# Optimization experiments

Hardware: AMD Instinct MI355X
Metric: run time of the kernel (lower is better)

## Reference

```python
import jax, jax.numpy as jnp
import numpy as np

F_, E_, B_, D_, H_, O_ = 4, 8, 4096, 512, 1024, 512


def setup_inputs() -> dict:
    key = jax.random.key(0)
    ks = jax.random.split(key, 7)
    s = 0.02  # small init scale to keep activations sane
    return {
        "features": jax.random.normal(ks[0], (F_, B_, D_), jnp.float32),
        "W1": jax.random.normal(ks[1], (F_, E_, D_, H_), jnp.float32) * s,
        "b1": jax.random.normal(ks[2], (F_, E_, H_), jnp.float32) * s,
        "W2": jax.random.normal(ks[3], (F_, E_, H_, O_), jnp.float32) * s,
        "b2": jax.random.normal(ks[4], (F_, E_, O_), jnp.float32) * s,
        "Wg": jax.random.normal(ks[5], (F_, D_, E_), jnp.float32) * s,
        "bg": jax.random.normal(ks[6], (F_, E_), jnp.float32) * s,
    }


def reference(features, W1, b1, W2, b2, Wg, bg):
    # Gate: softmax over experts, per feature. [F,B,E]
    gate = jax.nn.softmax(jnp.einsum('fbd,fde->fbe', features, Wg) + bg[:, None, :], axis=-1)
    # All experts computed densely (soft MoE): hidden [F,B,E,H]
    h = jax.nn.relu(jnp.einsum('fbd,fedh->fbeh', features, W1) + b1[:, None, :, :])
    # Expert outputs [F,B,E,O]
    eo = jnp.einsum('fbeh,feho->fbeo', h, W2) + b2[:, None, :, :]
    # Gate-weighted sum over experts, then mean over features -> [B,O]
    weighted = jnp.einsum('fbe,fbeo->fbo', gate, eo)
    return jnp.mean(weighted, axis=0)
```

## Files before the change

kernel.cpp:

```cpp
#include <hip/hip_runtime.h>


#define F_ 4
#define E_ 8
#define B_ 4096
#define D_ 512
#define H_ 1024
#define O_ 512

typedef unsigned short ushort_t;
typedef __bf16 bf16x8 __attribute__((ext_vector_type(8)));
typedef float f32x4 __attribute__((ext_vector_type(4)));
typedef unsigned short ushort8_t __attribute__((ext_vector_type(8)));

__device__ inline ushort_t f2bf(float f) {
  union { float f; unsigned u; } v; v.f = f;
  unsigned r = v.u + 0x7FFFu + ((v.u >> 16) & 1u);
  return (ushort_t)(r >> 16);
}
__device__ inline float bf2f(ushort_t u) {
  union { unsigned u; float f; } v; v.u = ((unsigned)u) << 16;
  return v.f;
}

__device__ inline void async16(const void* g, void* l) {
  __builtin_amdgcn_global_load_lds(
      (const __attribute__((address_space(1))) unsigned int*)g,
      (__attribute__((address_space(3))) unsigned int*)l, 16, 0, 0);
}

__device__ inline unsigned ldsOff(const void* p) {
  return (unsigned)(unsigned long long)(const __attribute__((address_space(3))) char*)p;
}
__device__ inline bf16x8 dsr128(unsigned byteOff) {
  bf16x8 r;
  asm volatile("ds_read_b128 %0, %1" : "=v"(r) : "v"(byteOff));
  return r;
}

#define VM0 asm volatile("s_waitcnt vmcnt(0)" ::: "memory")
#define VM6 asm volatile("s_waitcnt vmcnt(6)" ::: "memory")
#define BAR { __builtin_amdgcn_sched_barrier(0); __builtin_amdgcn_s_barrier(); \
              __builtin_amdgcn_sched_barrier(0); }

__global__ void prep_kernel(const float* __restrict__ features, const float* __restrict__ Wg,
                            const float* __restrict__ bg, float* __restrict__ g2,
                            ushort_t* __restrict__ featbf) {
  const int fb = blockIdx.x;
  const int f = fb >> 12, b = fb & (B_ - 1);
  const int lane = threadIdx.x;
  const float* feat = features + ((size_t)f * B_ + b) * D_;
  const float* wg = Wg + (size_t)f * D_ * E_;
  const int d0 = lane * 8;
  float ff[8];
  *(float4*)&ff[0] = *(const float4*)&feat[d0];
  *(float4*)&ff[4] = *(const float4*)&feat[d0 + 4];
  ushort8_t u;
#pragma unroll
  for (int k = 0; k < 8; ++k) u[k] = f2bf(ff[k]);
  *(ushort8_t*)&featbf[((size_t)f * B_ + b) * D_ + d0] = u;

  float acc[E_] = {0.f, 0.f, 0.f, 0.f, 0.f, 0.f, 0.f, 0.f};
#pragma unroll
  for (int k = 0; k < 8; ++k) {
    const float fv = ff[k];
    const float4 w0 = ((const float4*)(wg + (size_t)(d0 + k) * E_))[0];
    const float4 w1 = ((const float4*)(wg + (size_t)(d0 + k) * E_))[1];
    acc[0] += fv * w0.x; acc[1] += fv * w0.y; acc[2] += fv * w0.z; acc[3] += fv * w0.w;
    acc[4] += fv * w1.x; acc[5] += fv * w1.y; acc[6] += fv * w1.z; acc[7] += fv * w1.w;
  }
#pragma unroll
  for (int off = 32; off >= 1; off >>= 1)
#pragma unroll
    for (int e = 0; e < E_; ++e) acc[e] += __shfl_xor(acc[e], off, 64);
  float lg[E_], mx = -1e30f;
#pragma unroll
  for (int e = 0; e < E_; ++e) { lg[e] = acc[e] + bg[f * E_ + e]; mx = fmaxf(mx, lg[e]); }
  float s = 0.f;
#pragma unroll
  for (int e = 0; e < E_; ++e) { lg[e] = __expf(lg[e] - mx); s += lg[e]; }
  const float inv = 1.f / (s * (float)F_);
  if (lane < E_) g2[((size_t)f * B_ + b) * E_ + lane] = lg[lane] * inv;
}

__global__ void transpose_cast_kernel(const float* __restrict__ in, ushort_t* __restrict__ out,
                                      int R, int C) {
  __shared__ float tile[64][65];
  const size_t zoff = (size_t)blockIdx.z * R * C;
  in += zoff; out += zoff;
  const int tx = threadIdx.x & 63, ty = threadIdx.x >> 6;
  const int r0 = blockIdx.y * 64, c0 = blockIdx.x * 64;
#pragma unroll
  for (int i = 0; i < 16; ++i) {
    const int r = ty + i * 4;
    tile[r][tx] = in[(size_t)(r0 + r) * C + c0 + tx];
  }
  __syncthreads();
#pragma unroll
  for (int i = 0; i < 16; ++i) {
    const int c = ty + i * 4;
    out[(size_t)(c0 + c) * R + r0 + tx] = f2bf(tile[tx][c]);
  }
}


#define G1_STAGE(ktn, c) { \
    ushort_t* s_ = &lds[(c) * 32768]; \
    const ushort_t* a_ = aG + (ktn) * 64; \
    const ushort_t* b_ = bG + (ktn) * 64; \
    _Pragma("unroll") for (int p = 0; p < 4; ++p) { \
      async16(a_ + (size_t)p * (64 * D_), s_ + p * 4096 + t * 8); \
      async16(b_ + (size_t)p * (64 * D_), s_ + 16384 + p * 4096 + t * 8); } }

#define G1_PHASE(sb, kh) { \
    bf16x8 af[8], bfr[4]; \
    const unsigned cx = (unsigned)((((kh) * 4 + q) ^ (lr & 7)) * 16); \
    _Pragma("unroll") for (int i_ = 0; i_ < 8; ++i_) \
      af[i_] = dsr128((sb) + (unsigned)((wm * 128 + i_ * 16 + lr) * 128) + cx); \
    _Pragma("unroll") for (int j_ = 0; j_ < 4; ++j_) \
      bfr[j_] = dsr128((sb) + 32768u + (unsigned)((wn * 64 + j_ * 16 + lr) * 128) + cx); \
    asm volatile("s_waitcnt lgkmcnt(0)" ::: "memory"); \
    __builtin_amdgcn_sched_barrier(0); \
    __builtin_amdgcn_s_setprio(1); \
    _Pragma("unroll") for (int i_ = 0; i_ < 8; ++i_) \
      _Pragma("unroll") for (int j_ = 0; j_ < 4; ++j_) \
        acc[i_][j_] = __builtin_amdgcn_mfma_f32_16x16x32_bf16(bfr[j_], af[i_], acc[i_][j_], 0, 0, 0); \
    __builtin_amdgcn_s_setprio(0); \
    __builtin_amdgcn_sched_barrier(0); }

#define G1_ITER(kt, c) { \
    const unsigned sb = ldsB + (c) * 65536u; \
    G1_STAGE((kt) + 1, (c) ^ 1); \
    G1_PHASE(sb, 0); \
    G1_PHASE(sb, 1); \
    VM0; BAR; }

__global__ __launch_bounds__(512, 2) void gemm1_kernel(
    const ushort_t* __restrict__ featbf, const ushort_t* __restrict__ w1t,
    const float* __restrict__ b1, const float* __restrict__ g2,
    ushort_t* __restrict__ Hf, int f) {
  __shared__ __align__(16) ushort_t lds[65536];
  const int id = blockIdx.x;
  const int e = id & 7;
  const int s = id >> 3;
  const int n0 = (s & 3) * 256;
  const int m0 = (s >> 2) * 256;
  const ushort_t* A  = featbf + (size_t)f * B_ * D_;
  const ushort_t* Bp = w1t + ((size_t)f * E_ + e) * (size_t)H_ * D_;
  const float* b1e = b1 + ((size_t)f * E_ + e) * H_;
  const float* g2f = g2 + (size_t)f * B_ * E_;
  ushort_t* HfE = Hf + (size_t)e * B_ * H_;

  const int t = threadIdx.x, lane = t & 63, w = t >> 6;
  const int wm = w >> 2, wn = w & 3;
  const int lr = lane & 15, q = lane >> 4;
  const unsigned ldsB = ldsOff(lds);

  const int rr = t >> 3;
  const int cc = (t & 7) ^ (rr & 7);
  const ushort_t* aG = A  + (size_t)(m0 + rr) * D_ + cc * 8;
  const ushort_t* bG = Bp + (size_t)(n0 + rr) * D_ + cc * 8;

  f32x4 acc[8][4];
#pragma unroll
  for (int i = 0; i < 8; ++i)
#pragma unroll
    for (int j = 0; j < 4; ++j) acc[i][j] = (f32x4){0.f, 0.f, 0.f, 0.f};

  G1_STAGE(0, 0);
  VM0; BAR;

  G1_ITER(0, 0); G1_ITER(1, 1);
  G1_ITER(2, 0); G1_ITER(3, 1);
  G1_ITER(4, 0); G1_ITER(5, 1);
  G1_ITER(6, 0);
  { const unsigned sb = ldsB + 65536u;
    G1_PHASE(sb, 0); G1_PHASE(sb, 1); }

  __syncthreads();
  ushort_t* cb = lds;
#pragma unroll
  for (int mh = 0; mh < 2; ++mh) {
    if (wm == mh) {
#pragma unroll
      for (int i = 0; i < 8; ++i) {
        const int rl = i * 16 + lr;
        const float gv = g2f[(size_t)(m0 + mh * 128 + rl) * E_ + e];
#pragma unroll
        for (int j = 0; j < 4; ++j) {
          const int nl = wn * 64 + j * 16 + q * 4;
          const float4 bb = *(const float4*)&b1e[n0 + nl];
          ushort4 o;
          o.x = f2bf(fmaxf(acc[i][j][0] + bb.x, 0.f) * gv);
          o.y = f2bf(fmaxf(acc[i][j][1] + bb.y, 0.f) * gv);
          o.z = f2bf(fmaxf(acc[i][j][2] + bb.z, 0.f) * gv);
          o.w = f2bf(fmaxf(acc[i][j][3] + bb.w, 0.f) * gv);
          *(ushort4*)&cb[rl * 264 + nl] = o;
        }
      }
    }
    __syncthreads();
    const int row = t >> 2, seg = t & 3;
    const ushort_t* src = &cb[row * 264 + seg * 64];
    ushort_t* dst = HfE + (size_t)(m0 + mh * 128 + row) * H_ + n0 + seg * 64;
#pragma unroll
    for (int c2 = 0; c2 < 8; ++c2)
      *(ushort8_t*)(dst + c2 * 8) = *(const ushort8_t*)(src + c2 * 8);
    __syncthreads();
  }
}


#define G2_STAGE(ktn, c) { \
    ushort_t* s_ = &lds2[(c) * 24576]; \
    const ushort_t* a_ = Hf + (size_t)(e0 + ((ktn) >> 4)) * ((size_t)B_ * H_) + aOff + ((ktn) & 15) * 64; \
    const ushort_t* b_ = w2tF + (size_t)(e0 + ((ktn) >> 4)) * ((size_t)O_ * H_) + bOff + ((ktn) & 15) * 64; \
    _Pragma("unroll") for (int p = 0; p < 2; ++p) \
      async16(a_ + (size_t)p * (64 * H_), s_ + p * 4096 + t * 8); \
    _Pragma("unroll") for (int p = 0; p < 4; ++p) \
      async16(b_ + (size_t)p * (64 * H_), s_ + 8192 + p * 4096 + t * 8); }

#define G2_PHASE(sb, kh) { \
    bf16x8 af[4], bfr[4]; \
    const unsigned cx = (unsigned)((((kh) * 4 + q) ^ (lr & 7)) * 16); \
    _Pragma("unroll") for (int i_ = 0; i_ < 4; ++i_) \
      af[i_] = dsr128((sb) + (unsigned)((wm * 64 + i_ * 16 + lr) * 128) + cx); \
    _Pragma("unroll") for (int j_ = 0; j_ < 4; ++j_) \
      bfr[j_] = dsr128((sb) + 16384u + (unsigned)((wn * 64 + j_ * 16 + lr) * 128) + cx); \
    asm volatile("s_waitcnt lgkmcnt(0)" ::: "memory"); \
    __builtin_amdgcn_sched_barrier(0); \
    __builtin_amdgcn_s_setprio(1); \
    _Pragma("unroll") for (int i_ = 0; i_ < 4; ++i_) \
      _Pragma("unroll") for (int j_ = 0; j_ < 4; ++j_) \
        acc[i_][j_] = __builtin_amdgcn_mfma_f32_16x16x32_bf16(bfr[j_], af[i_], acc[i_][j_], 0, 0, 0); \
    __builtin_amdgcn_s_setprio(0); \
    __builtin_amdgcn_sched_barrier(0); }

#define G2_ITER(kt, c, cn) { \
    const unsigned sb = ldsB + (c) * 49152u; \
    G2_STAGE((kt) + 2, cn); \
    G2_PHASE(sb, 0); \
    G2_PHASE(sb, 1); \
    VM6; BAR; }

__global__ __launch_bounds__(512, 2) void gemm2_kernel(
    const ushort_t* __restrict__ Hf, const ushort_t* __restrict__ w2t,
    const float* __restrict__ b2, const float* __restrict__ g2,
    ushort_t* __restrict__ part, int f) {
  __shared__ __align__(16) ushort_t lds2[73728];
  const int id = blockIdx.x;
  const int grp = id & 3;
  const int s = id >> 2;
  const int n0 = (s & 1) * 256;
  const int m0 = (s >> 1) * 128;
  const int e0 = grp * 2;
  const ushort_t* w2tF = w2t + (size_t)f * E_ * O_ * H_;
  const float* g2f = g2 + (size_t)f * B_ * E_;

  const int t = threadIdx.x, lane = t & 63, w = t >> 6;
  const int wm = w >> 2, wn = w & 3;
  const int lr = lane & 15, q = lane >> 4;
  const unsigned ldsB = ldsOff(lds2);

  const int rr = t >> 3;
  const int cc = (t & 7) ^ (rr & 7);
  const size_t aOff = (size_t)(m0 + rr) * H_ + cc * 8;
  const size_t bOff = (size_t)(n0 + rr) * H_ + cc * 8;

  f32x4 acc[4][4];
#pragma unroll
  for (int i = 0; i < 4; ++i)
#pragma unroll
    for (int j = 0; j < 4; ++j) acc[i][j] = (f32x4){0.f, 0.f, 0.f, 0.f};

  G2_STAGE(0, 0); G2_STAGE(1, 1);
  VM6; BAR;

  for (int b = 0; b < 30; b += 3) {
    G2_ITER(b + 0, 0, 2);
    G2_ITER(b + 1, 1, 0);
    G2_ITER(b + 2, 2, 1);
  }
  { const unsigned sb = ldsB + 0u;
    G2_PHASE(sb, 0); G2_PHASE(sb, 1); VM0; BAR; }
  { const unsigned sb = ldsB + 49152u;
    G2_PHASE(sb, 0); G2_PHASE(sb, 1); }

  __syncthreads();
  ushort_t* cb = lds2;
  const float* b2e0 = b2 + ((size_t)f * E_ + e0) * O_;
  const float* b2e1 = b2e0 + O_;
#pragma unroll
  for (int i = 0; i < 4; ++i) {
    const int ml = wm * 64 + i * 16 + lr;
    const float gv0 = g2f[(size_t)(m0 + ml) * E_ + e0];
    const float gv1 = g2f[(size_t)(m0 + ml) * E_ + e0 + 1];
#pragma unroll
    for (int j = 0; j < 4; ++j) {
      const int nl = wn * 64 + j * 16 + q * 4;
      const int n = n0 + nl;
      const float4 c0 = *(const float4*)&b2e0[n];
      const float4 c1 = *(const float4*)&b2e1[n];
      ushort4 o;
      o.x = f2bf(acc[i][j][0] + gv0 * c0.x + gv1 * c1.x);
      o.y = f2bf(acc[i][j][1] + gv0 * c0.y + gv1 * c1.y);
      o.z = f2bf(acc[i][j][2] + gv0 * c0.z + gv1 * c1.z);
      o.w = f2bf(acc[i][j][3] + gv0 * c0.w + gv1 * c1.w);
      *(ushort4*)&cb[ml * 264 + nl] = o;
    }
  }
  __syncthreads();
  const int row = t >> 2, seg = t & 3;
  const ushort_t* src = &cb[row * 264 + seg * 64];
  ushort_t* dst = part + (size_t)(f * 4 + grp) * (B_ * O_) + (size_t)(m0 + row) * O_ + n0 + seg * 64;
#pragma unroll
  for (int c2 = 0; c2 < 8; ++c2)
    *(ushort8_t*)(dst + c2 * 8) = *(const ushort8_t*)(src + c2 * 8);
}

__global__ void reduce_kernel(const ushort_t* __restrict__ part, float* __restrict__ out) {
  const size_t p = ((size_t)blockIdx.x * 256 + threadIdx.x) * 8;
  float s[8] = {0.f, 0.f, 0.f, 0.f, 0.f, 0.f, 0.f, 0.f};
#pragma unroll
  for (int k = 0; k < F_ * 4; ++k) {
    const ushort8_t u = *(const ushort8_t*)&part[(size_t)k * (B_ * O_) + p];
#pragma unroll
    for (int j = 0; j < 8; ++j) s[j] += bf2f(u[j]);
  }
  float4 o0 = {s[0], s[1], s[2], s[3]}, o1 = {s[4], s[5], s[6], s[7]};
  *(float4*)&out[p] = o0;
  *(float4*)&out[p + 4] = o1;
}

extern "C" void kernel_launch(void* const* d_in, const int* in_sizes, int n_in,
                              void* d_out, int out_size, void* d_ws, size_t ws_size,
                              hipStream_t stream) {
  const float* features = (const float*)d_in[0];
  const float* W1 = (const float*)d_in[1];
  const float* b1 = (const float*)d_in[2];
  const float* W2 = (const float*)d_in[3];
  const float* b2 = (const float*)d_in[4];
  const float* Wg = (const float*)d_in[5];
  const float* bg = (const float*)d_in[6];
  float* out = (float*)d_out;

  char* ws = (char*)d_ws;
  ushort_t* featbf = (ushort_t*)ws;
  ushort_t* w1t    = (ushort_t*)(ws + 16777216);
  ushort_t* w2t    = (ushort_t*)(ws + 50331648);
  float*    g2     = (float*)(ws + 83886080);
  ushort_t* Hf     = (ushort_t*)(ws + 84410368);
  ushort_t* part   = (ushort_t*)(ws + 151519232);

  prep_kernel<<<F_ * B_, 64, 0, stream>>>(features, Wg, bg, g2, featbf);
  transpose_cast_kernel<<<dim3(H_ / 64, D_ / 64, F_ * E_), 256, 0, stream>>>(W1, w1t, D_, H_);
  transpose_cast_kernel<<<dim3(O_ / 64, H_ / 64, F_ * E_), 256, 0, stream>>>(W2, w2t, H_, O_);

  for (int f = 0; f < F_; ++f) {
    gemm1_kernel<<<512, 512, 0, stream>>>(featbf, w1t, b1, g2, Hf, f);
    gemm2_kernel<<<256, 512, 0, stream>>>(Hf, w2t, b2, g2, part, f);
  }
  reduce_kernel<<<B_ * O_ / 8 / 256, 256, 0, stream>>>(part, out);
}
```

Measured before the change: 621.6 us.

## Restructure GEMM pipelines into half-K phases with per-phase staging and new warp layout

Both GEMM kernels now load K in 32-wide half-tiles. Each half-tile gets its own async stage and a barrier before it is read, and the next stage's loads are issued between the LDS reads and the MFMAs. Partial vmcnt waits replace the full drains. The warp grid changes from 2x4 to 4x2, the LDS swizzle is rebuilt for 64-byte rows, and gemm2's block tile goes from 128x256 to 256x128 with a smaller LDS footprint. The aim is finer-grained overlap of global loads with compute and less LDS, in exchange for more barriers per K step.

```diff
diff --git a/kernel.cpp b/kernel.cpp
--- a/kernel.cpp
+++ b/kernel.cpp
@@ -38,10 +38,12 @@
   return r;
 }
 
+#define LGKM0 asm volatile("s_waitcnt lgkmcnt(0)" ::: "memory")
+#define VM4 asm volatile("s_waitcnt vmcnt(4)" ::: "memory")
+#define VM3 asm volatile("s_waitcnt vmcnt(3)" ::: "memory")
 #define VM0 asm volatile("s_waitcnt vmcnt(0)" ::: "memory")
-#define VM6 asm volatile("s_waitcnt vmcnt(6)" ::: "memory")
-#define BAR { __builtin_amdgcn_sched_barrier(0); __builtin_amdgcn_s_barrier(); \
-              __builtin_amdgcn_sched_barrier(0); }
+#define SCB __builtin_amdgcn_sched_barrier(0)
+#define SBAR __builtin_amdgcn_s_barrier()
 
 __global__ void prep_kernel(const float* __restrict__ features, const float* __restrict__ Wg,
                             const float* __restrict__ bg, float* __restrict__ g2,
@@ -104,36 +106,28 @@
 }
 
 
-#define G1_STAGE(ktn, c) { \
-    ushort_t* s_ = &lds[(c) * 32768]; \
-    const ushort_t* a_ = aG + (ktn) * 64; \
-    const ushort_t* b_ = bG + (ktn) * 64; \
-    _Pragma("unroll") for (int p = 0; p < 4; ++p) { \
-      async16(a_ + (size_t)p * (64 * D_), s_ + p * 4096 + t * 8); \
-      async16(b_ + (size_t)p * (64 * D_), s_ + 16384 + p * 4096 + t * 8); } }
-
-#define G1_PHASE(sb, kh) { \
-    bf16x8 af[8], bfr[4]; \
-    const unsigned cx = (unsigned)((((kh) * 4 + q) ^ (lr & 7)) * 16); \
-    _Pragma("unroll") for (int i_ = 0; i_ < 8; ++i_) \
-      af[i_] = dsr128((sb) + (unsigned)((wm * 128 + i_ * 16 + lr) * 128) + cx); \
-    _Pragma("unroll") for (int j_ = 0; j_ < 4; ++j_) \
-      bfr[j_] = dsr128((sb) + 32768u + (unsigned)((wn * 64 + j_ * 16 + lr) * 128) + cx); \
-    asm volatile("s_waitcnt lgkmcnt(0)" ::: "memory"); \
-    __builtin_amdgcn_sched_barrier(0); \
+#define STG1(ktn, kh) { \
+    char* d_ = (char*)lds + (((ktn) & 1) << 16) + (kh) * 16384 + t * 16; \
+    const int ko_ = (ktn) * 64 + (kh) * 32; \
+    async16(aT + ko_, d_); \
+    async16(aT + 128 * D_ + ko_, d_ + 8192); \
+    async16(bT + ko_, d_ + 32768); \
+    async16(bT + 128 * D_ + ko_, d_ + 40960); }
+
+#define PH1(kt, kh, DOSTG, VMS) { \
+    VMS; \
+    asm volatile("" ::: "memory"); SBAR; SCB; \
+    const unsigned sb_ = ldsB + (unsigned)(((kt) & 1) << 16) + (kh) * 16384u; \
+    bf16x8 af[4], bfr[8]; \
+    _Pragma("unroll") for (int i_ = 0; i_ < 4; ++i_) af[i_] = dsr128(sb_ + aRd + i_ * 1024u); \
+    _Pragma("unroll") for (int j_ = 0; j_ < 8; ++j_) bfr[j_] = dsr128(sb_ + 32768u + bRd + j_ * 1024u); \
+    if (DOSTG) { STG1((kt) + 1, kh); } \
+    LGKM0; SCB; \
     __builtin_amdgcn_s_setprio(1); \
-    _Pragma("unroll") for (int i_ = 0; i_ < 8; ++i_) \
-      _Pragma("unroll") for (int j_ = 0; j_ < 4; ++j_) \
+    _Pragma("unroll") for (int i_ = 0; i_ < 4; ++i_) \
+      _Pragma("unroll") for (int j_ = 0; j_ < 8; ++j_) \
         acc[i_][j_] = __builtin_amdgcn_mfma_f32_16x16x32_bf16(bfr[j_], af[i_], acc[i_][j_], 0, 0, 0); \
-    __builtin_amdgcn_s_setprio(0); \
-    __builtin_amdgcn_sched_barrier(0); }
-
-#define G1_ITER(kt, c) { \
-    const unsigned sb = ldsB + (c) * 65536u; \
-    G1_STAGE((kt) + 1, (c) ^ 1); \
-    G1_PHASE(sb, 0); \
-    G1_PHASE(sb, 1); \
-    VM0; BAR; }
+    __builtin_amdgcn_s_setprio(0); SCB; }
 
 __global__ __launch_bounds__(512, 2) void gemm1_kernel(
     const ushort_t* __restrict__ featbf, const ushort_t* __restrict__ w1t,
@@ -145,50 +139,50 @@
   const int s = id >> 3;
   const int n0 = (s & 3) * 256;
   const int m0 = (s >> 2) * 256;
-  const ushort_t* A  = featbf + (size_t)f * B_ * D_;
-  const ushort_t* Bp = w1t + ((size_t)f * E_ + e) * (size_t)H_ * D_;
   const float* b1e = b1 + ((size_t)f * E_ + e) * H_;
   const float* g2f = g2 + (size_t)f * B_ * E_;
   ushort_t* HfE = Hf + (size_t)e * B_ * H_;
 
   const int t = threadIdx.x, lane = t & 63, w = t >> 6;
-  const int wm = w >> 2, wn = w & 3;
+  const int wm = w >> 1, wn = w & 1;
   const int lr = lane & 15, q = lane >> 4;
   const unsigned ldsB = ldsOff(lds);
-
-  const int rr = t >> 3;
-  const int cc = (t & 7) ^ (rr & 7);
-  const ushort_t* aG = A  + (size_t)(m0 + rr) * D_ + cc * 8;
-  const ushort_t* bG = Bp + (size_t)(n0 + rr) * D_ + cc * 8;
-
-  f32x4 acc[8][4];
-#pragma unroll
-  for (int i = 0; i < 8; ++i)
-#pragma unroll
-    for (int j = 0; j < 4; ++j) acc[i][j] = (f32x4){0.f, 0.f, 0.f, 0.f};
-
-  G1_STAGE(0, 0);
-  VM0; BAR;
-
-  G1_ITER(0, 0); G1_ITER(1, 1);
-  G1_ITER(2, 0); G1_ITER(3, 1);
-  G1_ITER(4, 0); G1_ITER(5, 1);
-  G1_ITER(6, 0);
-  { const unsigned sb = ldsB + 65536u;
-    G1_PHASE(sb, 0); G1_PHASE(sb, 1); }
-
-  __syncthreads();
+  const unsigned csw = (unsigned)((q ^ ((lr >> 1) & 3)) << 4);
+  const unsigned aRd = (unsigned)((wm * 64 + lr) * 64) + csw;
+  const unsigned bRd = (unsigned)((wn * 128 + lr) * 64) + csw;
+
+  const int cc = (t & 3) ^ ((t >> 3) & 3);
+  const ushort_t* aT = featbf + (size_t)f * B_ * D_ + (size_t)(m0 + (t >> 2)) * D_ + cc * 8;
+  const ushort_t* bT = w1t + ((size_t)f * E_ + e) * ((size_t)H_ * D_) +
+                       (size_t)(n0 + (t >> 2)) * D_ + cc * 8;
+
+  f32x4 acc[4][8];
+#pragma unroll
+  for (int i = 0; i < 4; ++i)
+#pragma unroll
+    for (int j = 0; j < 8; ++j) acc[i][j] = (f32x4){0.f, 0.f, 0.f, 0.f};
+
+  STG1(0, 0); STG1(0, 1);
+
+  for (int kt = 0; kt < 7; ++kt) {
+    PH1(kt, 0, true, VM4);
+    PH1(kt, 1, true, VM4);
+  }
+  PH1(7, 0, false, VM4);
+  PH1(7, 1, false, VM0);
+
+  asm volatile("" ::: "memory"); SBAR; SCB;
   ushort_t* cb = lds;
 #pragma unroll
   for (int mh = 0; mh < 2; ++mh) {
-    if (wm == mh) {
-#pragma unroll
-      for (int i = 0; i < 8; ++i) {
-        const int rl = i * 16 + lr;
+    if ((wm >> 1) == mh) {
+#pragma unroll
+      for (int i = 0; i < 4; ++i) {
+        const int rl = (wm & 1) * 64 + i * 16 + lr;
         const float gv = g2f[(size_t)(m0 + mh * 128 + rl) * E_ + e];
 #pragma unroll
-        for (int j = 0; j < 4; ++j) {
-          const int nl = wn * 64 + j * 16 + q * 4;
+        for (int j = 0; j < 8; ++j) {
+          const int nl = wn * 128 + j * 16 + q * 4;
           const float4 bb = *(const float4*)&b1e[n0 + nl];
           ushort4 o;
           o.x = f2bf(fmaxf(acc[i][j][0] + bb.x, 0.f) * gv);
@@ -200,72 +194,72 @@
       }
     }
     __syncthreads();
-    const int row = t >> 2, seg = t & 3;
-    const ushort_t* src = &cb[row * 264 + seg * 64];
-    ushort_t* dst = HfE + (size_t)(m0 + mh * 128 + row) * H_ + n0 + seg * 64;
-#pragma unroll
-    for (int c2 = 0; c2 < 8; ++c2)
-      *(ushort8_t*)(dst + c2 * 8) = *(const ushort8_t*)(src + c2 * 8);
+    {
+      const int row = t >> 2, seg = t & 3;
+      const ushort_t* src = &cb[row * 264 + seg * 64];
+      ushort_t* dst = HfE + (size_t)(m0 + mh * 128 + row) * H_ + n0 + seg * 64;
+#pragma unroll
+      for (int c2 = 0; c2 < 8; ++c2)
+        *(ushort8_t*)(dst + c2 * 8) = *(const ushort8_t*)(src + c2 * 8);
+    }
     __syncthreads();
   }
 }
 
 
-#define G2_STAGE(ktn, c) { \
-    ushort_t* s_ = &lds2[(c) * 24576]; \
-    const ushort_t* a_ = Hf + (size_t)(e0 + ((ktn) >> 4)) * ((size_t)B_ * H_) + aOff + ((ktn) & 15) * 64; \
-    const ushort_t* b_ = w2tF + (size_t)(e0 + ((ktn) >> 4)) * ((size_t)O_ * H_) + bOff + ((ktn) & 15) * 64; \
-    _Pragma("unroll") for (int p = 0; p < 2; ++p) \
-      async16(a_ + (size_t)p * (64 * H_), s_ + p * 4096 + t * 8); \
-    _Pragma("unroll") for (int p = 0; p < 4; ++p) \
-      async16(b_ + (size_t)p * (64 * H_), s_ + 8192 + p * 4096 + t * 8); }
-
-#define G2_PHASE(sb, kh) { \
+#define STG2(ktn, kh) { \
+    const size_t eo_ = (size_t)((ktn) >> 4); \
+    const int ko_ = ((ktn) & 15) * 64 + (kh) * 32; \
+    const ushort_t* a_ = aT + eo_ * ((size_t)B_ * H_) + ko_; \
+    const ushort_t* b_ = bT + eo_ * ((size_t)O_ * H_) + ko_; \
+    char* dA_ = (char*)lds + (((ktn) & 1) ? 49152 : 0) + (kh) * 16384 + t * 16; \
+    char* dB_ = (char*)lds + (((ktn) & 1) ? 49152 : 0) + 32768 + (kh) * 8192 + t * 16; \
+    async16(a_, dA_); \
+    async16(a_ + 128 * H_, dA_ + 8192); \
+    async16(b_, dB_); }
+
+#define PH2(kt, kh, DOSTG, VMS) { \
+    VMS; \
+    asm volatile("" ::: "memory"); SBAR; SCB; \
+    const unsigned sb_ = ldsB + (unsigned)(((kt) & 1) ? 49152 : 0); \
     bf16x8 af[4], bfr[4]; \
-    const unsigned cx = (unsigned)((((kh) * 4 + q) ^ (lr & 7)) * 16); \
     _Pragma("unroll") for (int i_ = 0; i_ < 4; ++i_) \
-      af[i_] = dsr128((sb) + (unsigned)((wm * 64 + i_ * 16 + lr) * 128) + cx); \
+      af[i_] = dsr128(sb_ + (kh) * 16384u + aRd + i_ * 1024u); \
     _Pragma("unroll") for (int j_ = 0; j_ < 4; ++j_) \
-      bfr[j_] = dsr128((sb) + 16384u + (unsigned)((wn * 64 + j_ * 16 + lr) * 128) + cx); \
-    asm volatile("s_waitcnt lgkmcnt(0)" ::: "memory"); \
-    __builtin_amdgcn_sched_barrier(0); \
+      bfr[j_] = dsr128(sb_ + 32768u + (kh) * 8192u + bRd + j_ * 1024u); \
+    if (DOSTG) { STG2((kt) + 1, kh); } \
+    LGKM0; SCB; \
     __builtin_amdgcn_s_setprio(1); \
     _Pragma("unroll") for (int i_ = 0; i_ < 4; ++i_) \
       _Pragma("unroll") for (int j_ = 0; j_ < 4; ++j_) \
         acc[i_][j_] = __builtin_amdgcn_mfma_f32_16x16x32_bf16(bfr[j_], af[i_], acc[i_][j_], 0, 0, 0); \
-    __builtin_amdgcn_s_setprio(0); \
-    __builtin_amdgcn_sched_barrier(0); }
-
-#define G2_ITER(kt, c, cn) { \
-    const unsigned sb = ldsB + (c) * 49152u; \
-    G2_STAGE((kt) + 2, cn); \
-    G2_PHASE(sb, 0); \
-    G2_PHASE(sb, 1); \
-    VM6; BAR; }
+    __builtin_amdgcn_s_setprio(0); SCB; }
 
 __global__ __launch_bounds__(512, 2) void gemm2_kernel(
     const ushort_t* __restrict__ Hf, const ushort_t* __restrict__ w2t,
     const float* __restrict__ b2, const float* __restrict__ g2,
     ushort_t* __restrict__ part, int f) {
-  __shared__ __align__(16) ushort_t lds2[73728];
+  __shared__ __align__(16) ushort_t lds[49152];
   const int id = blockIdx.x;
   const int grp = id & 3;
   const int s = id >> 2;
-  const int n0 = (s & 1) * 256;
-  const int m0 = (s >> 1) * 128;
+  const int n0 = (s & 3) * 128;
+  const int m0 = (s >> 2) * 256;
   const int e0 = grp * 2;
-  const ushort_t* w2tF = w2t + (size_t)f * E_ * O_ * H_;
   const float* g2f = g2 + (size_t)f * B_ * E_;
 
   const int t = threadIdx.x, lane = t & 63, w = t >> 6;
-  const int wm = w >> 2, wn = w & 3;
+  const int wm = w >> 1, wn = w & 1;
   const int lr = lane & 15, q = lane >> 4;
-  const unsigned ldsB = ldsOff(lds2);
-
-  const int rr = t >> 3;
-  const int cc = (t & 7) ^ (rr & 7);
-  const size_t aOff = (size_t)(m0 + rr) * H_ + cc * 8;
-  const size_t bOff = (size_t)(n0 + rr) * H_ + cc * 8;
+  const unsigned ldsB = ldsOff(lds);
+  const unsigned csw = (unsigned)((q ^ ((lr >> 1) & 3)) << 4);
+  const unsigned aRd = (unsigned)((wm * 64 + lr) * 64) + csw;
+  const unsigned bRd = (unsigned)((wn * 64 + lr) * 64) + csw;
+
+  const int cc = (t & 3) ^ ((t >> 3) & 3);
+  const ushort_t* aT = Hf + (size_t)e0 * B_ * H_ + (size_t)(m0 + (t >> 2)) * H_ + cc * 8;
+  const ushort_t* bT = w2t + ((size_t)f * E_ + e0) * ((size_t)O_ * H_) +
+                       (size_t)(n0 + (t >> 2)) * H_ + cc * 8;
 
   f32x4 acc[4][4];
 #pragma unroll
@@ -273,49 +267,54 @@
 #pragma unroll
     for (int j = 0; j < 4; ++j) acc[i][j] = (f32x4){0.f, 0.f, 0.f, 0.f};
 
-  G2_STAGE(0, 0); G2_STAGE(1, 1);
-  VM6; BAR;
-
-  for (int b = 0; b < 30; b += 3) {
-    G2_ITER(b + 0, 0, 2);
-    G2_ITER(b + 1, 1, 0);
-    G2_ITER(b + 2, 2, 1);
-  }
-  { const unsigned sb = ldsB + 0u;
-    G2_PHASE(sb, 0); G2_PHASE(sb, 1); VM0; BAR; }
-  { const unsigned sb = ldsB + 49152u;
-    G2_PHASE(sb, 0); G2_PHASE(sb, 1); }
-
-  __syncthreads();
-  ushort_t* cb = lds2;
+  STG2(0, 0); STG2(0, 1);
+
+  for (int kt = 0; kt < 31; ++kt) {
+    PH2(kt, 0, true, VM3);
+    PH2(kt, 1, true, VM3);
+  }
+  PH2(31, 0, false, VM3);
+  PH2(31, 1, false, VM0);
+
+  asm volatile("" ::: "memory"); SBAR; SCB;
+  ushort_t* cb = lds;
   const float* b2e0 = b2 + ((size_t)f * E_ + e0) * O_;
   const float* b2e1 = b2e0 + O_;
-#pragma unroll
-  for (int i = 0; i < 4; ++i) {
-    const int ml = wm * 64 + i * 16 + lr;
-    const float gv0 = g2f[(size_t)(m0 + ml) * E_ + e0];
-    const float gv1 = g2f[(size_t)(m0 + ml) * E_ + e0 + 1];
-#pragma unroll
-    for (int j = 0; j < 4; ++j) {
-      const int nl = wn * 64 + j * 16 + q * 4;
-      const int n = n0 + nl;
-      const float4 c0 = *(const float4*)&b2e0[n];
-      const float4 c1 = *(const float4*)&b2e1[n];
-      ushort4 o;
-      o.x = f2bf(acc[i][j][0] + gv0 * c0.x + gv1 * c1.x);
-      o.y = f2bf(acc[i][j][1] + gv0 * c0.y + gv1 * c1.y);
-      o.z = f2bf(acc[i][j][2] + gv0 * c0.z + gv1 * c1.z);
-      o.w = f2bf(acc[i][j][3] + gv0 * c0.w + gv1 * c1.w);
-      *(ushort4*)&cb[ml * 264 + nl] = o;
+  ushort_t* dstP = part + (size_t)(f * 4 + grp) * ((size_t)B_ * O_);
+#pragma unroll
+  for (int mh = 0; mh < 2; ++mh) {
+    if ((wm >> 1) == mh) {
+#pragma unroll
+      for (int i = 0; i < 4; ++i) {
+        const int rl = (wm & 1) * 64 + i * 16 + lr;
+        const size_t gr = (size_t)(m0 + mh * 128 + rl) * E_ + e0;
+        const float gv0 = g2f[gr], gv1 = g2f[gr + 1];
+#pragma unroll
+        for (int j = 0; j < 4; ++j) {
+          const int nl = wn * 64 + j * 16 + q * 4;
+          const int n = n0 + nl;
+          const float4 c0 = *(const float4*)&b2e0[n];
+          const float4 c1 = *(const float4*)&b2e1[n];
+          ushort4 o;
+          o.x = f2bf(acc[i][j][0] + gv0 * c0.x + gv1 * c1.x);
+          o.y = f2bf(acc[i][j][1] + gv0 * c0.y + gv1 * c1.y);
+          o.z = f2bf(acc[i][j][2] + gv0 * c0.z + gv1 * c1.z);
+          o.w = f2bf(acc[i][j][3] + gv0 * c0.w + gv1 * c1.w);
+          *(ushort4*)&cb[rl * 136 + nl] = o;
+        }
+      }
     }
-  }
-  __syncthreads();
-  const int row = t >> 2, seg = t & 3;
-  const ushort_t* src = &cb[row * 264 + seg * 64];
-  ushort_t* dst = part + (size_t)(f * 4 + grp) * (B_ * O_) + (size_t)(m0 + row) * O_ + n0 + seg * 64;
-#pragma unroll
-  for (int c2 = 0; c2 < 8; ++c2)
-    *(ushort8_t*)(dst + c2 * 8) = *(const ushort8_t*)(src + c2 * 8);
+    __syncthreads();
+    {
+      const int row = t >> 2, seg = t & 3;
+      const ushort_t* src = &cb[row * 136 + seg * 32];
+      ushort_t* dst = dstP + (size_t)(m0 + mh * 128 + row) * O_ + n0 + seg * 32;
+#pragma unroll
+      for (int c2 = 0; c2 < 4; ++c2)
+        *(ushort8_t*)(dst + c2 * 8) = *(const ushort8_t*)(src + c2 * 8);
+    }
+    __syncthreads();
+  }
 }
 
 __global__ void reduce_kernel(const ushort_t* __restrict__ part, float* __restrict__ out) {
```

New measurement: 655.9 us. 1.06x slower.
